# Performance work log

Hardware: AMD Instinct MI355X
Metric: run time of the kernel (lower is better)

Reference implementation:

```python
import jax, jax.numpy as jnp
import numpy as np

N = 50000      # nodes
F_IN = 128     # num_feat
HID = 128      # hidden size
OUT = 47       # num_out (classes)
E = 600000     # graph edges
EGO_E = 1200000  # concatenated egonet edges


def _linear_params(key, fan_in, fan_out):
    s = 1.0 / np.sqrt(fan_in)
    kw, kb = jax.random.split(key)
    W = jax.random.uniform(kw, (fan_in, fan_out), jnp.float32, -s, s)
    b = jax.random.uniform(kb, (fan_out,), jnp.float32, -s, s)
    return W, b


def setup_inputs() -> dict:
    key = jax.random.key(0)
    ks = jax.random.split(key, 8)
    x_in = jax.random.normal(ks[0], (N, F_IN), jnp.float32)
    edge_index_in = jax.random.randint(ks[1], (2, E), 0, N)
    ego_edge_index = jax.random.randint(ks[2], (2, EGO_E), 0, N)
    W_ego0, b_ego0 = _linear_params(ks[3], F_IN, F_IN)
    W_gin0, b_gin0 = _linear_params(ks[4], F_IN, HID)
    W_ego1, b_ego1 = _linear_params(ks[5], HID, HID)
    W_gin1, b_gin1 = _linear_params(ks[6], HID, OUT)
    return {
        "x_in": x_in, "edge_index_in": edge_index_in, "ego_edge_index": ego_edge_index,
        "W_ego0": W_ego0, "b_ego0": b_ego0, "W_gin0": W_gin0, "b_gin0": b_gin0,
        "W_ego1": W_ego1, "b_ego1": b_ego1, "W_gin1": W_gin1, "b_gin1": b_gin1,
    }


def reference(x_in, edge_index_in, ego_edge_index,
              W_ego0, b_ego0, W_gin0, b_gin0,
              W_ego1, b_ego1, W_gin1, b_gin1):
    n = x_in.shape[0]
    ego_row, ego_col = ego_edge_index[0], ego_edge_index[1]
    src, tgt = edge_index_in[0], edge_index_in[1]

    def do_conv(x):
        # sum_i spmm(A_i, x) == scatter-add over concatenated egonet edges, then / N
        return jax.ops.segment_sum(x[ego_col], ego_row, num_segments=n) * (1.0 / n)

    def gin(x, W, b):
        # GINConv(nn=Linear), eps=0: Linear(x + sum_{j->i} x_j)
        aggr = jax.ops.segment_sum(x[src], tgt, num_segments=n)
        return (x + aggr) @ W + b

    # layer 0: ['Ego','GIN', relu_mid=True, relu_end=True]
    x = do_conv(x_in) @ W_ego0 + b_ego0
    x = jax.nn.relu(x)
    x = gin(x, W_gin0, b_gin0)
    x = jax.nn.relu(x)
    # layer 1: ['Ego','GIN', relu_mid=True, relu_end=False]
    x = do_conv(x) @ W_ego1 + b_ego1
    x = jax.nn.relu(x)
    x = gin(x, W_gin1, b_gin1)
    return jax.nn.log_softmax(x, axis=1)
```

## Files before the change

kernel.cpp:

```cpp
#include <hip/hip_runtime.h>

#define SCAP_EGO 8192
#define SCAP_E   4096

typedef unsigned short ushort_t;
typedef unsigned int uint_t;
typedef __attribute__((ext_vector_type(8))) short bf16x8;
typedef __attribute__((ext_vector_type(4))) float f32x4;

__device__ inline float lo16(uint_t u) { return __uint_as_float(u << 16); }
__device__ inline float hi16(uint_t u) { return __uint_as_float(u & 0xFFFF0000u); }
__device__ inline ushort_t f2bf(float f) {
    uint_t i = __float_as_uint(f);
    return (ushort_t)((i + 0x7FFFu + ((i >> 16) & 1u)) >> 16);
}
__device__ inline uint_t pack2(float a, float b) {
    return (uint_t)f2bf(a) | ((uint_t)f2bf(b) << 16);
}

__global__ __launch_bounds__(256) void prep(
    const float* __restrict__ x, ushort_t* __restrict__ xb, int n8,
    const float* __restrict__ W0, const float* __restrict__ W1,
    const float* __restrict__ W2, const float* __restrict__ W3,
    ushort_t* __restrict__ T0, ushort_t* __restrict__ T1,
    ushort_t* __restrict__ T2, ushort_t* __restrict__ T3,
    int* __restrict__ z)
{
    int i = blockIdx.x * 256 + threadIdx.x;
    if (i < 128) ((int4*)z)[i] = make_int4(0, 0, 0, 0);
    if (i < n8) {
        const float4* p = (const float4*)(x + (size_t)i * 8);
        float4 a = p[0], b = p[1];
        uint4 o;
        o.x = pack2(a.x, a.y); o.y = pack2(a.z, a.w);
        o.z = pack2(b.x, b.y); o.w = pack2(b.z, b.w);
        *(uint4*)(xb + (size_t)i * 8) = o;
    }
    if (i < 49152) {
        int mi = i >> 14;
        int r = i & 16383;
        int n = r >> 7, k = r & 127;
        const float* W = mi == 0 ? W0 : (mi == 1 ? W1 : W2);
        ushort_t* T = mi == 0 ? T0 : (mi == 1 ? T1 : T2);
        T[n * 128 + k] = f2bf(W[k * 128 + n]);
    } else if (i < 49152 + 6144) {
        int r = i - 49152;
        int n = r >> 7, k = r & 127;
        T3[n * 128 + k] = (n < 47) ? f2bf(W3[k * 47 + n]) : (ushort_t)0;
    }
}

__global__ __launch_bounds__(256) void bin_edges2(
    const int* __restrict__ d1, const int* __restrict__ s1, int n1, int nb1,
    int* __restrict__ cur1, int2* __restrict__ st1, int scap1,
    const int* __restrict__ d2, const int* __restrict__ s2, int n2,
    int* __restrict__ cur2, int2* __restrict__ st2, int scap2)
{
    const int* dst; const int* src; int nE, scap; int* bincur; int2* stage; int bid;
    if (blockIdx.x < (uint_t)nb1) {
        dst = d1; src = s1; nE = n1; scap = scap1; bincur = cur1; stage = st1;
        bid = blockIdx.x;
    } else {
        dst = d2; src = s2; nE = n2; scap = scap2; bincur = cur2; stage = st2;
        bid = blockIdx.x - nb1;
    }
    __shared__ int bcnt[256];
    __shared__ int gbase[256];
    int t = threadIdx.x;
    bcnt[t] = 0;
    __syncthreads();
    int base = bid * 4096;
    int d[16], s[16], l[16];
#pragma unroll
    for (int i = 0; i < 16; i++) {
        int e = base + t + i * 256;
        if (e < nE) {
            d[i] = dst[e]; s[i] = src[e];
            l[i] = atomicAdd(&bcnt[d[i] >> 8], 1);
        } else d[i] = -1;
    }
    __syncthreads();
    if (bcnt[t]) gbase[t] = atomicAdd(&bincur[t], bcnt[t]);
    __syncthreads();
#pragma unroll
    for (int i = 0; i < 16; i++) {
        if (d[i] >= 0) {
            int b = d[i] >> 8;
            int slot = gbase[b] + l[i];
            if (slot < scap) stage[(size_t)b * scap + slot] = make_int2(d[i], s[i]);
        }
    }
}

__global__ __launch_bounds__(256) void build_csr2(
    const int* __restrict__ cur1, const int2* __restrict__ st1, int scap1,
    int* __restrict__ cnt1, int* __restrict__ rp1, int* __restrict__ pk1,
    const int* __restrict__ cur2, const int2* __restrict__ st2, int scap2,
    int* __restrict__ cnt2, int* __restrict__ rp2, int* __restrict__ pk2,
    int NB)
{
    const int* bincur; const int2* stage; int scap;
    int* cnt; int* rowptr; int* packed; int b;
    if (blockIdx.x < (uint_t)NB) {
        bincur = cur1; stage = st1; scap = scap1;
        cnt = cnt1; rowptr = rp1; packed = pk1; b = blockIdx.x;
    } else {
        bincur = cur2; stage = st2; scap = scap2;
        cnt = cnt2; rowptr = rp2; packed = pk2; b = blockIdx.x - NB;
    }
    __shared__ int sc[256];
    __shared__ int wcur[256];
    int t = threadIdx.x;
    int m = bincur[b]; if (m > scap) m = scap;
    const int2* st = stage + (size_t)b * scap;
    sc[t] = 0;
    __syncthreads();
    for (int e = t; e < m; e += 256) atomicAdd(&sc[st[e].x & 255], 1);
    __syncthreads();
    int v = sc[t];
    __syncthreads();
    sc[t] = v;
    __syncthreads();
    for (int off = 1; off < 256; off <<= 1) {
        int y = (t >= off) ? sc[t - off] : 0;
        __syncthreads();
        sc[t] += y;
        __syncthreads();
    }
    int excl = sc[t] - v;
    cnt[b * 256 + t] = v;
    rowptr[b * 256 + t] = b * scap + excl;
    wcur[t] = excl;
    __syncthreads();
    int* pk = packed + (size_t)b * scap;
    for (int e = t; e < m; e += 256) {
        int2 p = st[e];
        int slot = atomicAdd(&wcur[p.x & 255], 1);
        pk[slot] = p.y;
    }
}

template<int SELF>
__global__ __launch_bounds__(256, 8) void fused16(
    const ushort_t* __restrict__ X,
    const int* __restrict__ cnt, const int* __restrict__ rowptr,
    const int* __restrict__ packed,
    const ushort_t* __restrict__ WT, const float* __restrict__ bias,
    ushort_t* __restrict__ outb, int nrows, float scale)
{
    __shared__ ushort_t As[16][136];
    int t = threadIdx.x;
    int g = t >> 4, lane = t & 15;
    int blockBase = blockIdx.x * 16;
    int n = blockBase + g;
    const ushort_t* base = X + lane * 8;
    float a[8];
#pragma unroll
    for (int i = 0; i < 8; i++) a[i] = 0.f;
    if (n < nrows) {
        int len = cnt[n];
        const int* row = packed + rowptr[n];
        int e = 0;
        for (; e + 3 < len; e += 4) {
            uint4 w0 = *(const uint4*)(base + (size_t)row[e] * 128);
            uint4 w1 = *(const uint4*)(base + (size_t)row[e + 1] * 128);
            uint4 w2 = *(const uint4*)(base + (size_t)row[e + 2] * 128);
            uint4 w3 = *(const uint4*)(base + (size_t)row[e + 3] * 128);
            a[0] += lo16(w0.x) + lo16(w1.x) + lo16(w2.x) + lo16(w3.x);
            a[1] += hi16(w0.x) + hi16(w1.x) + hi16(w2.x) + hi16(w3.x);
            a[2] += lo16(w0.y) + lo16(w1.y) + lo16(w2.y) + lo16(w3.y);
            a[3] += hi16(w0.y) + hi16(w1.y) + hi16(w2.y) + hi16(w3.y);
            a[4] += lo16(w0.z) + lo16(w1.z) + lo16(w2.z) + lo16(w3.z);
            a[5] += hi16(w0.z) + hi16(w1.z) + hi16(w2.z) + hi16(w3.z);
            a[6] += lo16(w0.w) + lo16(w1.w) + lo16(w2.w) + lo16(w3.w);
            a[7] += hi16(w0.w) + hi16(w1.w) + hi16(w2.w) + hi16(w3.w);
        }
        for (; e < len; e++) {
            uint4 w = *(const uint4*)(base + (size_t)row[e] * 128);
            a[0] += lo16(w.x); a[1] += hi16(w.x);
            a[2] += lo16(w.y); a[3] += hi16(w.y);
            a[4] += lo16(w.z); a[5] += hi16(w.z);
            a[6] += lo16(w.w); a[7] += hi16(w.w);
        }
        if (SELF) {
            uint4 w = *(const uint4*)(base + (size_t)n * 128);
            a[0] += lo16(w.x); a[1] += hi16(w.x);
            a[2] += lo16(w.y); a[3] += hi16(w.y);
            a[4] += lo16(w.z); a[5] += hi16(w.z);
            a[6] += lo16(w.w); a[7] += hi16(w.w);
        }
    }
    uint4 o;
    o.x = pack2(a[0] * scale, a[1] * scale);
    o.y = pack2(a[2] * scale, a[3] * scale);
    o.z = pack2(a[4] * scale, a[5] * scale);
    o.w = pack2(a[6] * scale, a[7] * scale);
    *(uint4*)&As[g][lane * 8] = o;
    __syncthreads();
    int wave = t >> 6, l64 = t & 63;
    int m = l64 & 15, quad = l64 >> 4;
    bf16x8 afr[4];
#pragma unroll
    for (int kt = 0; kt < 4; kt++)
        afr[kt] = *(const bf16x8*)&As[m][kt * 32 + quad * 8];
    f32x4 acc[2];
#pragma unroll
    for (int j = 0; j < 2; j++) acc[j] = (f32x4){0.f, 0.f, 0.f, 0.f};
#pragma unroll
    for (int j = 0; j < 2; j++) {
        int ct = wave * 2 + j;
#pragma unroll
        for (int kt = 0; kt < 4; kt++) {
            bf16x8 b = *(const bf16x8*)(WT + (size_t)(ct * 16 + m) * 128
                                           + kt * 32 + quad * 8);
            acc[j] = __builtin_amdgcn_mfma_f32_16x16x32_bf16(afr[kt], b, acc[j], 0, 0, 0);
        }
    }
#pragma unroll
    for (int j = 0; j < 2; j++) {
        int col = (wave * 2 + j) * 16 + m;
        float bb = bias[col];
#pragma unroll
        for (int r = 0; r < 4; r++) {
            int row = blockBase + quad * 4 + r;
            if (row < nrows) {
                float v = acc[j][r] + bb;
                v = fmaxf(v, 0.f);
                outb[(size_t)row * 128 + col] = f2bf(v);
            }
        }
    }
}

__global__ __launch_bounds__(256, 8) void fused47(
    const ushort_t* __restrict__ X,
    const int* __restrict__ cnt, const int* __restrict__ rowptr,
    const int* __restrict__ packed,
    const ushort_t* __restrict__ WT, const float* __restrict__ bias,
    float* __restrict__ out, int nrows)
{
    __shared__ ushort_t As[16][136];
    int t = threadIdx.x;
    int g = t >> 4, lane = t & 15;
    int blockBase = blockIdx.x * 16;
    int n = blockBase + g;
    const ushort_t* base = X + lane * 8;
    float a[8];
#pragma unroll
    for (int i = 0; i < 8; i++) a[i] = 0.f;
    if (n < nrows) {
        int len = cnt[n];
        const int* row = packed + rowptr[n];
        int e = 0;
        for (; e + 3 < len; e += 4) {
            uint4 w0 = *(const uint4*)(base + (size_t)row[e] * 128);
            uint4 w1 = *(const uint4*)(base + (size_t)row[e + 1] * 128);
            uint4 w2 = *(const uint4*)(base + (size_t)row[e + 2] * 128);
            uint4 w3 = *(const uint4*)(base + (size_t)row[e + 3] * 128);
            a[0] += lo16(w0.x) + lo16(w1.x) + lo16(w2.x) + lo16(w3.x);
            a[1] += hi16(w0.x) + hi16(w1.x) + hi16(w2.x) + hi16(w3.x);
            a[2] += lo16(w0.y) + lo16(w1.y) + lo16(w2.y) + lo16(w3.y);
            a[3] += hi16(w0.y) + hi16(w1.y) + hi16(w2.y) + hi16(w3.y);
            a[4] += lo16(w0.z) + lo16(w1.z) + lo16(w2.z) + lo16(w3.z);
            a[5] += hi16(w0.z) + hi16(w1.z) + hi16(w2.z) + hi16(w3.z);
            a[6] += lo16(w0.w) + lo16(w1.w) + lo16(w2.w) + lo16(w3.w);
            a[7] += hi16(w0.w) + hi16(w1.w) + hi16(w2.w) + hi16(w3.w);
        }
        for (; e < len; e++) {
            uint4 w = *(const uint4*)(base + (size_t)row[e] * 128);
            a[0] += lo16(w.x); a[1] += hi16(w.x);
            a[2] += lo16(w.y); a[3] += hi16(w.y);
            a[4] += lo16(w.z); a[5] += hi16(w.z);
            a[6] += lo16(w.w); a[7] += hi16(w.w);
        }
        uint4 w = *(const uint4*)(base + (size_t)n * 128);
        a[0] += lo16(w.x); a[1] += hi16(w.x);
        a[2] += lo16(w.y); a[3] += hi16(w.y);
        a[4] += lo16(w.z); a[5] += hi16(w.z);
        a[6] += lo16(w.w); a[7] += hi16(w.w);
    }
    uint4 o;
    o.x = pack2(a[0], a[1]);
    o.y = pack2(a[2], a[3]);
    o.z = pack2(a[4], a[5]);
    o.w = pack2(a[6], a[7]);
    *(uint4*)&As[g][lane * 8] = o;
    __syncthreads();
    int wave = t >> 6;
    if (wave != 0) return;
    int l64 = t & 63;
    int m = l64 & 15, quad = l64 >> 4;
    bf16x8 afr[4];
#pragma unroll
    for (int kt = 0; kt < 4; kt++)
        afr[kt] = *(const bf16x8*)&As[m][kt * 32 + quad * 8];
    f32x4 acc[3];
#pragma unroll
    for (int ct = 0; ct < 3; ct++) acc[ct] = (f32x4){0.f, 0.f, 0.f, 0.f};
#pragma unroll
    for (int ct = 0; ct < 3; ct++) {
#pragma unroll
        for (int kt = 0; kt < 4; kt++) {
            bf16x8 b = *(const bf16x8*)(WT + (size_t)(ct * 16 + m) * 128
                                           + kt * 32 + quad * 8);
            acc[ct] = __builtin_amdgcn_mfma_f32_16x16x32_bf16(afr[kt], b, acc[ct], 0, 0, 0);
        }
    }
    int c0 = m, c1 = 16 + m, c2 = 32 + m;
    bool has2 = (c2 < 47);
    float b0 = bias[c0], b1 = bias[c1], b2 = has2 ? bias[c2] : 0.f;
#pragma unroll
    for (int r = 0; r < 4; r++) {
        int row = blockBase + quad * 4 + r;
        float v0 = acc[0][r] + b0;
        float v1 = acc[1][r] + b1;
        float v2 = has2 ? (acc[2][r] + b2) : -INFINITY;
        float mx = fmaxf(fmaxf(v0, v1), v2);
#pragma unroll
        for (int off = 8; off; off >>= 1) mx = fmaxf(mx, __shfl_xor(mx, off, 64));
        float s = __expf(v0 - mx) + __expf(v1 - mx) + (has2 ? __expf(v2 - mx) : 0.f);
#pragma unroll
        for (int off = 8; off; off >>= 1) s += __shfl_xor(s, off, 64);
        float lse = mx + __logf(s);
        if (row < nrows) {
            float* o2 = out + (size_t)row * 47;
            o2[c0] = v0 - lse;
            o2[c1] = v1 - lse;
            if (has2) o2[c2] = v2 - lse;
        }
    }
}

extern "C" void kernel_launch(void* const* d_in, const int* in_sizes, int n_in,
                              void* d_out, int out_size, void* d_ws, size_t ws_size,
                              hipStream_t stream) {
    const float* x_in   = (const float*)d_in[0];
    const int*   edge   = (const int*)d_in[1];
    const int*   ego    = (const int*)d_in[2];
    const float* W_ego0 = (const float*)d_in[3];
    const float* b_ego0 = (const float*)d_in[4];
    const float* W_gin0 = (const float*)d_in[5];
    const float* b_gin0 = (const float*)d_in[6];
    const float* W_ego1 = (const float*)d_in[7];
    const float* b_ego1 = (const float*)d_in[8];
    const float* W_gin1 = (const float*)d_in[9];
    const float* b_gin1 = (const float*)d_in[10];
    float* out = (float*)d_out;

    const int N     = in_sizes[0] / 128;
    const int E     = in_sizes[1] / 2;
    const int EGO_E = in_sizes[2] / 2;
    const float invN = 1.0f / (float)N;
    const int NB    = (N + 255) >> 8;

    const size_t NBELEM = (size_t)N * 128;
    ushort_t* Xb = (ushort_t*)d_ws;
    ushort_t* G  = Xb + NBELEM;
    ushort_t* H  = G + NBELEM;
    ushort_t* T0 = H + NBELEM;
    ushort_t* T1 = T0 + 16384;
    ushort_t* T2 = T1 + 16384;
    ushort_t* T3 = T2 + 16384;
    int* ip = (int*)(T3 + 6144);
    int* cnt_ego   = ip;             ip += NB * 256;
    int* rp_ego    = ip;             ip += NB * 256;
    int* cnt_edge  = ip;             ip += NB * 256;
    int* rp_edge   = ip;             ip += NB * 256;
    int* bincur    = ip;             ip += 512;
    int2* stage_ego  = (int2*)ip;    ip += (size_t)NB * SCAP_EGO * 2;
    int*  pk_ego     = ip;           ip += (size_t)NB * SCAP_EGO;
    int2* stage_edge = (int2*)ip;    ip += (size_t)NB * SCAP_E * 2;
    int*  pk_edge    = ip;           ip += (size_t)NB * SCAP_E;

    const int gFused  = (N + 15) / 16;
    const int gBinE   = (EGO_E + 4095) / 4096;
    const int gBinF   = (E + 4095) / 4096;
    const int gCvt    = ((N * 128 / 8) + 255) / 256;

    prep<<<gCvt, 256, 0, stream>>>(x_in, Xb, N * 128 / 8,
                                   W_ego0, W_gin0, W_ego1, W_gin1,
                                   T0, T1, T2, T3, bincur);
    bin_edges2<<<gBinE + gBinF, 256, 0, stream>>>(
        ego, ego + EGO_E, EGO_E, gBinE, bincur, stage_ego, SCAP_EGO,
        edge + E, edge, E, bincur + 256, stage_edge, SCAP_E);
    build_csr2<<<2 * NB, 256, 0, stream>>>(
        bincur, stage_ego, SCAP_EGO, cnt_ego, rp_ego, pk_ego,
        bincur + 256, stage_edge, SCAP_E, cnt_edge, rp_edge, pk_edge, NB);

    fused16<0><<<gFused, 256, 0, stream>>>(Xb, cnt_ego, rp_ego, pk_ego,
                                           T0, b_ego0, H, N, invN);
    fused16<1><<<gFused, 256, 0, stream>>>(H, cnt_edge, rp_edge, pk_edge,
                                           T1, b_gin0, G, N, 1.f);
    fused16<0><<<gFused, 256, 0, stream>>>(G, cnt_ego, rp_ego, pk_ego,
                                           T2, b_ego1, H, N, invN);
    fused47<<<gFused, 256, 0, stream>>>(H, cnt_edge, rp_edge, pk_edge,
                                        T3, b_gin1, out, N);
}
```

Baseline: 300.7 us.

## Fuse all pipeline stages into one persistent cooperative kernel with grid syncs

Replaces the seven separate launches (prep, edge binning, CSR build, and the four aggregate-plus-matmul stages) with a single cooperative kernel. Blocks loop over work items and separate stages with grid.sync. The grid size comes from the occupancy query, capped at 2048 blocks. This is meant to remove per-launch overhead and the tail idle time at kernel boundaries, at the cost of grid-wide barriers, one register budget shared by every stage (possible spills in the binning code under the 8-blocks-per-CU bound), and a fallback multi-kernel path if the cooperative launch fails.

```diff
diff --git a/kernel.cpp b/kernel.cpp
--- a/kernel.cpp
+++ b/kernel.cpp
@@ -1,4 +1,7 @@
 #include <hip/hip_runtime.h>
+#include <hip/hip_cooperative_groups.h>
+
+namespace cg = cooperative_groups;
 
 #define SCAP_EGO 8192
 #define SCAP_E   4096
@@ -18,7 +21,8 @@
     return (uint_t)f2bf(a) | ((uint_t)f2bf(b) << 16);
 }
 
-__global__ __launch_bounds__(256) void prep(
+
+__device__ __forceinline__ void dev_prep_item(int i,
     const float* __restrict__ x, ushort_t* __restrict__ xb, int n8,
     const float* __restrict__ W0, const float* __restrict__ W1,
     const float* __restrict__ W2, const float* __restrict__ W3,
@@ -26,7 +30,6 @@
     ushort_t* __restrict__ T2, ushort_t* __restrict__ T3,
     int* __restrict__ z)
 {
-    int i = blockIdx.x * 256 + threadIdx.x;
     if (i < 128) ((int4*)z)[i] = make_int4(0, 0, 0, 0);
     if (i < n8) {
         const float4* p = (const float4*)(x + (size_t)i * 8);
@@ -50,23 +53,21 @@
     }
 }
 
-__global__ __launch_bounds__(256) void bin_edges2(
-    const int* __restrict__ d1, const int* __restrict__ s1, int n1, int nb1,
-    int* __restrict__ cur1, int2* __restrict__ st1, int scap1,
+__device__ __forceinline__ void dev_bin_chunk(int c, int nc1,
+    const int* __restrict__ d1, const int* __restrict__ s1, int n1,
+    int2* __restrict__ st1, int* __restrict__ cur1, int scap1,
     const int* __restrict__ d2, const int* __restrict__ s2, int n2,
-    int* __restrict__ cur2, int2* __restrict__ st2, int scap2)
+    int2* __restrict__ st2, int* __restrict__ cur2, int scap2,
+    int* bcnt, int* gbase, int t)
 {
     const int* dst; const int* src; int nE, scap; int* bincur; int2* stage; int bid;
-    if (blockIdx.x < (uint_t)nb1) {
+    if (c < nc1) {
         dst = d1; src = s1; nE = n1; scap = scap1; bincur = cur1; stage = st1;
-        bid = blockIdx.x;
+        bid = c;
     } else {
         dst = d2; src = s2; nE = n2; scap = scap2; bincur = cur2; stage = st2;
-        bid = blockIdx.x - nb1;
-    }
-    __shared__ int bcnt[256];
-    __shared__ int gbase[256];
-    int t = threadIdx.x;
+        bid = c - nc1;
+    }
     bcnt[t] = 0;
     __syncthreads();
     int base = bid * 4096;
@@ -90,27 +91,25 @@
             if (slot < scap) stage[(size_t)b * scap + slot] = make_int2(d[i], s[i]);
         }
     }
-}
-
-__global__ __launch_bounds__(256) void build_csr2(
+    __syncthreads();
+}
+
+__device__ __forceinline__ void dev_csr_bin(int c, int NB,
     const int* __restrict__ cur1, const int2* __restrict__ st1, int scap1,
     int* __restrict__ cnt1, int* __restrict__ rp1, int* __restrict__ pk1,
     const int* __restrict__ cur2, const int2* __restrict__ st2, int scap2,
     int* __restrict__ cnt2, int* __restrict__ rp2, int* __restrict__ pk2,
-    int NB)
+    int* sc, int* wcur, int t)
 {
     const int* bincur; const int2* stage; int scap;
     int* cnt; int* rowptr; int* packed; int b;
-    if (blockIdx.x < (uint_t)NB) {
+    if (c < NB) {
         bincur = cur1; stage = st1; scap = scap1;
-        cnt = cnt1; rowptr = rp1; packed = pk1; b = blockIdx.x;
+        cnt = cnt1; rowptr = rp1; packed = pk1; b = c;
     } else {
         bincur = cur2; stage = st2; scap = scap2;
-        cnt = cnt2; rowptr = rp2; packed = pk2; b = blockIdx.x - NB;
-    }
-    __shared__ int sc[256];
-    __shared__ int wcur[256];
-    int t = threadIdx.x;
+        cnt = cnt2; rowptr = rp2; packed = pk2; b = c - NB;
+    }
     int m = bincur[b]; if (m > scap) m = scap;
     const int2* st = stage + (size_t)b * scap;
     sc[t] = 0;
@@ -134,24 +133,23 @@
     __syncthreads();
     int* pk = packed + (size_t)b * scap;
     for (int e = t; e < m; e += 256) {
-        int2 p = st[e];
-        int slot = atomicAdd(&wcur[p.x & 255], 1);
-        pk[slot] = p.y;
-    }
-}
-
-template<int SELF>
-__global__ __launch_bounds__(256, 8) void fused16(
+        int2 p2 = st[e];
+        int slot = atomicAdd(&wcur[p2.x & 255], 1);
+        pk[slot] = p2.y;
+    }
+    __syncthreads();
+}
+
+__device__ __forceinline__ void dev_f16(int tile, int SELF,
     const ushort_t* __restrict__ X,
     const int* __restrict__ cnt, const int* __restrict__ rowptr,
     const int* __restrict__ packed,
     const ushort_t* __restrict__ WT, const float* __restrict__ bias,
-    ushort_t* __restrict__ outb, int nrows, float scale)
-{
-    __shared__ ushort_t As[16][136];
-    int t = threadIdx.x;
+    ushort_t* __restrict__ outb, int nrows, float scale,
+    ushort_t As[16][136], int t)
+{
     int g = t >> 4, lane = t & 15;
-    int blockBase = blockIdx.x * 16;
+    int blockBase = tile * 16;
     int n = blockBase + g;
     const ushort_t* base = X + lane * 8;
     float a[8];
@@ -230,19 +228,19 @@
             }
         }
     }
-}
-
-__global__ __launch_bounds__(256, 8) void fused47(
+    __syncthreads();
+}
+
+__device__ __forceinline__ void dev_f47(int tile,
     const ushort_t* __restrict__ X,
     const int* __restrict__ cnt, const int* __restrict__ rowptr,
     const int* __restrict__ packed,
     const ushort_t* __restrict__ WT, const float* __restrict__ bias,
-    float* __restrict__ out, int nrows)
-{
-    __shared__ ushort_t As[16][136];
-    int t = threadIdx.x;
+    float* __restrict__ out, int nrows,
+    ushort_t As[16][136], int t)
+{
     int g = t >> 4, lane = t & 15;
-    int blockBase = blockIdx.x * 16;
+    int blockBase = tile * 16;
     int n = blockBase + g;
     const ushort_t* base = X + lane * 8;
     float a[8];
@@ -287,48 +285,153 @@
     *(uint4*)&As[g][lane * 8] = o;
     __syncthreads();
     int wave = t >> 6;
-    if (wave != 0) return;
-    int l64 = t & 63;
-    int m = l64 & 15, quad = l64 >> 4;
-    bf16x8 afr[4];
-#pragma unroll
-    for (int kt = 0; kt < 4; kt++)
-        afr[kt] = *(const bf16x8*)&As[m][kt * 32 + quad * 8];
-    f32x4 acc[3];
-#pragma unroll
-    for (int ct = 0; ct < 3; ct++) acc[ct] = (f32x4){0.f, 0.f, 0.f, 0.f};
-#pragma unroll
-    for (int ct = 0; ct < 3; ct++) {
-#pragma unroll
-        for (int kt = 0; kt < 4; kt++) {
-            bf16x8 b = *(const bf16x8*)(WT + (size_t)(ct * 16 + m) * 128
-                                           + kt * 32 + quad * 8);
-            acc[ct] = __builtin_amdgcn_mfma_f32_16x16x32_bf16(afr[kt], b, acc[ct], 0, 0, 0);
-        }
-    }
-    int c0 = m, c1 = 16 + m, c2 = 32 + m;
-    bool has2 = (c2 < 47);
-    float b0 = bias[c0], b1 = bias[c1], b2 = has2 ? bias[c2] : 0.f;
-#pragma unroll
-    for (int r = 0; r < 4; r++) {
-        int row = blockBase + quad * 4 + r;
-        float v0 = acc[0][r] + b0;
-        float v1 = acc[1][r] + b1;
-        float v2 = has2 ? (acc[2][r] + b2) : -INFINITY;
-        float mx = fmaxf(fmaxf(v0, v1), v2);
-#pragma unroll
-        for (int off = 8; off; off >>= 1) mx = fmaxf(mx, __shfl_xor(mx, off, 64));
-        float s = __expf(v0 - mx) + __expf(v1 - mx) + (has2 ? __expf(v2 - mx) : 0.f);
-#pragma unroll
-        for (int off = 8; off; off >>= 1) s += __shfl_xor(s, off, 64);
-        float lse = mx + __logf(s);
-        if (row < nrows) {
-            float* o2 = out + (size_t)row * 47;
-            o2[c0] = v0 - lse;
-            o2[c1] = v1 - lse;
-            if (has2) o2[c2] = v2 - lse;
-        }
-    }
+    if (wave == 0) {
+        int l64 = t & 63;
+        int m = l64 & 15, quad = l64 >> 4;
+        bf16x8 afr[4];
+#pragma unroll
+        for (int kt = 0; kt < 4; kt++)
+            afr[kt] = *(const bf16x8*)&As[m][kt * 32 + quad * 8];
+        f32x4 acc[3];
+#pragma unroll
+        for (int ct = 0; ct < 3; ct++) acc[ct] = (f32x4){0.f, 0.f, 0.f, 0.f};
+#pragma unroll
+        for (int ct = 0; ct < 3; ct++) {
+#pragma unroll
+            for (int kt = 0; kt < 4; kt++) {
+                bf16x8 b = *(const bf16x8*)(WT + (size_t)(ct * 16 + m) * 128
+                                               + kt * 32 + quad * 8);
+                acc[ct] = __builtin_amdgcn_mfma_f32_16x16x32_bf16(afr[kt], b, acc[ct], 0, 0, 0);
+            }
+        }
+        int c0 = m, c1 = 16 + m, c2 = 32 + m;
+        bool has2 = (c2 < 47);
+        float b0 = bias[c0], b1 = bias[c1], b2 = has2 ? bias[c2] : 0.f;
+#pragma unroll
+        for (int r = 0; r < 4; r++) {
+            int row = blockBase + quad * 4 + r;
+            float v0 = acc[0][r] + b0;
+            float v1 = acc[1][r] + b1;
+            float v2 = has2 ? (acc[2][r] + b2) : -INFINITY;
+            float mx = fmaxf(fmaxf(v0, v1), v2);
+#pragma unroll
+            for (int off = 8; off; off >>= 1) mx = fmaxf(mx, __shfl_xor(mx, off, 64));
+            float s = __expf(v0 - mx) + __expf(v1 - mx) + (has2 ? __expf(v2 - mx) : 0.f);
+#pragma unroll
+            for (int off = 8; off; off >>= 1) s += __shfl_xor(s, off, 64);
+            float lse = mx + __logf(s);
+            if (row < nrows) {
+                float* o2 = out + (size_t)row * 47;
+                o2[c0] = v0 - lse;
+                o2[c1] = v1 - lse;
+                if (has2) o2[c2] = v2 - lse;
+            }
+        }
+    }
+    __syncthreads();
+}
+
+struct MegaP {
+    const float* x_in; const int* edge; const int* ego;
+    const float *W0, *W1, *W2, *W3;
+    const float *bE0, *bG0, *bE1, *bG1;
+    float* out;
+    ushort_t *Xb, *G, *H, *T0, *T1, *T2, *T3;
+    int *cnt_ego, *rp_ego, *pk_ego, *cnt_edge, *rp_edge, *pk_edge, *bincur;
+    int2 *st_ego, *st_edge;
+    int N, E, EGO_E, NB, n8; float invN;
+};
+
+__global__ __launch_bounds__(256, 8) void mega(MegaP p)
+{
+    cg::grid_group grid = cg::this_grid();
+    __shared__ int sA[256], sB[256];
+    __shared__ ushort_t As[16][136];
+    int t = threadIdx.x, bid = blockIdx.x, nb = gridDim.x;
+    int gsz = nb * 256, tix = bid * 256 + t;
+
+    for (int i = tix; i < p.n8; i += gsz)
+        dev_prep_item(i, p.x_in, p.Xb, p.n8, p.W0, p.W1, p.W2, p.W3,
+                      p.T0, p.T1, p.T2, p.T3, p.bincur);
+    grid.sync();
+
+    int nc1 = (p.EGO_E + 4095) >> 12, nc2 = (p.E + 4095) >> 12;
+    for (int c = bid; c < nc1 + nc2; c += nb)
+        dev_bin_chunk(c, nc1,
+                      p.ego, p.ego + p.EGO_E, p.EGO_E, p.st_ego, p.bincur, SCAP_EGO,
+                      p.edge + p.E, p.edge, p.E, p.st_edge, p.bincur + 256, SCAP_E,
+                      sA, sB, t);
+    grid.sync();
+
+    for (int c = bid; c < 2 * p.NB; c += nb)
+        dev_csr_bin(c, p.NB,
+                    p.bincur, p.st_ego, SCAP_EGO, p.cnt_ego, p.rp_ego, p.pk_ego,
+                    p.bincur + 256, p.st_edge, SCAP_E, p.cnt_edge, p.rp_edge, p.pk_edge,
+                    sA, sB, t);
+    grid.sync();
+
+    int nt = (p.N + 15) >> 4;
+    for (int tile = bid; tile < nt; tile += nb)
+        dev_f16(tile, 0, p.Xb, p.cnt_ego, p.rp_ego, p.pk_ego,
+                p.T0, p.bE0, p.H, p.N, p.invN, As, t);
+    grid.sync();
+    for (int tile = bid; tile < nt; tile += nb)
+        dev_f16(tile, 1, p.H, p.cnt_edge, p.rp_edge, p.pk_edge,
+                p.T1, p.bG0, p.G, p.N, 1.f, As, t);
+    grid.sync();
+    for (int tile = bid; tile < nt; tile += nb)
+        dev_f16(tile, 0, p.G, p.cnt_ego, p.rp_ego, p.pk_ego,
+                p.T2, p.bE1, p.H, p.N, p.invN, As, t);
+    grid.sync();
+    for (int tile = bid; tile < nt; tile += nb)
+        dev_f47(tile, p.H, p.cnt_edge, p.rp_edge, p.pk_edge,
+                p.T3, p.bG1, p.out, p.N, As, t);
+}
+
+__global__ __launch_bounds__(256) void k_prep(
+    const float* x, ushort_t* xb, int n8,
+    const float* W0, const float* W1, const float* W2, const float* W3,
+    ushort_t* T0, ushort_t* T1, ushort_t* T2, ushort_t* T3, int* z)
+{
+    int i = blockIdx.x * 256 + threadIdx.x;
+    dev_prep_item(i, x, xb, n8, W0, W1, W2, W3, T0, T1, T2, T3, z);
+}
+
+__global__ __launch_bounds__(256) void k_bin(
+    const int* d1, const int* s1, int n1, int nb1, int* cur1, int2* st1, int scap1,
+    const int* d2, const int* s2, int n2, int* cur2, int2* st2, int scap2)
+{
+    __shared__ int bcnt[256], gbase[256];
+    dev_bin_chunk(blockIdx.x, nb1, d1, s1, n1, st1, cur1, scap1,
+                  d2, s2, n2, st2, cur2, scap2, bcnt, gbase, threadIdx.x);
+}
+
+__global__ __launch_bounds__(256) void k_csr(
+    const int* cur1, const int2* st1, int scap1, int* cnt1, int* rp1, int* pk1,
+    const int* cur2, const int2* st2, int scap2, int* cnt2, int* rp2, int* pk2,
+    int NB)
+{
+    __shared__ int sc[256], wcur[256];
+    dev_csr_bin(blockIdx.x, NB, cur1, st1, scap1, cnt1, rp1, pk1,
+                cur2, st2, scap2, cnt2, rp2, pk2, sc, wcur, threadIdx.x);
+}
+
+__global__ __launch_bounds__(256, 8) void k_f16(
+    const ushort_t* X, const int* cnt, const int* rp, const int* pk,
+    const ushort_t* WT, const float* bias, ushort_t* outb, int nrows,
+    float scale, int SELF)
+{
+    __shared__ ushort_t As[16][136];
+    dev_f16(blockIdx.x, SELF, X, cnt, rp, pk, WT, bias, outb, nrows, scale,
+            As, threadIdx.x);
+}
+
+__global__ __launch_bounds__(256, 8) void k_f47(
+    const ushort_t* X, const int* cnt, const int* rp, const int* pk,
+    const ushort_t* WT, const float* bias, float* out, int nrows)
+{
+    __shared__ ushort_t As[16][136];
+    dev_f47(blockIdx.x, X, cnt, rp, pk, WT, bias, out, nrows, As, threadIdx.x);
 }
 
 extern "C" void kernel_launch(void* const* d_in, const int* in_sizes, int n_in,
@@ -352,6 +455,7 @@
     const int EGO_E = in_sizes[2] / 2;
     const float invN = 1.0f / (float)N;
     const int NB    = (N + 255) >> 8;
+    const int n8    = N * 128 / 8;
 
     const size_t NBELEM = (size_t)N * 128;
     ushort_t* Xb = (ushort_t*)d_ws;
@@ -372,27 +476,61 @@
     int2* stage_edge = (int2*)ip;    ip += (size_t)NB * SCAP_E * 2;
     int*  pk_edge    = ip;           ip += (size_t)NB * SCAP_E;
 
-    const int gFused  = (N + 15) / 16;
-    const int gBinE   = (EGO_E + 4095) / 4096;
-    const int gBinF   = (E + 4095) / 4096;
-    const int gCvt    = ((N * 128 / 8) + 255) / 256;
-
-    prep<<<gCvt, 256, 0, stream>>>(x_in, Xb, N * 128 / 8,
-                                   W_ego0, W_gin0, W_ego1, W_gin1,
-                                   T0, T1, T2, T3, bincur);
-    bin_edges2<<<gBinE + gBinF, 256, 0, stream>>>(
-        ego, ego + EGO_E, EGO_E, gBinE, bincur, stage_ego, SCAP_EGO,
-        edge + E, edge, E, bincur + 256, stage_edge, SCAP_E);
-    build_csr2<<<2 * NB, 256, 0, stream>>>(
-        bincur, stage_ego, SCAP_EGO, cnt_ego, rp_ego, pk_ego,
-        bincur + 256, stage_edge, SCAP_E, cnt_edge, rp_edge, pk_edge, NB);
-
-    fused16<0><<<gFused, 256, 0, stream>>>(Xb, cnt_ego, rp_ego, pk_ego,
-                                           T0, b_ego0, H, N, invN);
-    fused16<1><<<gFused, 256, 0, stream>>>(H, cnt_edge, rp_edge, pk_edge,
-                                           T1, b_gin0, G, N, 1.f);
-    fused16<0><<<gFused, 256, 0, stream>>>(G, cnt_ego, rp_ego, pk_ego,
-                                           T2, b_ego1, H, N, invN);
-    fused47<<<gFused, 256, 0, stream>>>(H, cnt_edge, rp_edge, pk_edge,
-                                        T3, b_gin1, out, N);
-}
+    MegaP P;
+    P.x_in = x_in; P.edge = edge; P.ego = ego;
+    P.W0 = W_ego0; P.W1 = W_gin0; P.W2 = W_ego1; P.W3 = W_gin1;
+    P.bE0 = b_ego0; P.bG0 = b_gin0; P.bE1 = b_ego1; P.bG1 = b_gin1;
+    P.out = out;
+    P.Xb = Xb; P.G = G; P.H = H;
+    P.T0 = T0; P.T1 = T1; P.T2 = T2; P.T3 = T3;
+    P.cnt_ego = cnt_ego; P.rp_ego = rp_ego; P.pk_ego = pk_ego;
+    P.cnt_edge = cnt_edge; P.rp_edge = rp_edge; P.pk_edge = pk_edge;
+    P.bincur = bincur; P.st_ego = stage_ego; P.st_edge = stage_edge;
+    P.N = N; P.E = E; P.EGO_E = EGO_E; P.NB = NB; P.n8 = n8; P.invN = invN;
+
+    static int coopGrid = 0;
+    if (coopGrid == 0) {
+        int dev = 0; (void)hipGetDevice(&dev);
+        hipDeviceProp_t prop;
+        int nCU = 256;
+        if (hipGetDeviceProperties(&prop, dev) == hipSuccess &&
+            prop.multiProcessorCount > 0)
+            nCU = prop.multiProcessorCount;
+        int mab = 0;
+        if (hipOccupancyMaxActiveBlocksPerMultiprocessor(&mab, mega, 256, 0)
+                != hipSuccess || mab < 1)
+            mab = 1;
+        long g = (long)mab * nCU;
+        if (g > 2048) g = 2048;
+        coopGrid = (int)g;
+    }
+
+    void* kargs[] = { (void*)&P };
+    hipError_t err = hipLaunchCooperativeKernel((const void*)mega,
+                                                dim3(coopGrid), dim3(256),
+                                                kargs, 0, stream);
+    if (err != hipSuccess) {
+        (void)hipGetLastError();
+        const int gFused = (N + 15) / 16;
+        const int gBinE  = (EGO_E + 4095) / 4096;
+        const int gBinF  = (E + 4095) / 4096;
+        const int gCvt   = (n8 + 255) / 256;
+        k_prep<<<gCvt, 256, 0, stream>>>(x_in, Xb, n8,
+                                         W_ego0, W_gin0, W_ego1, W_gin1,
+                                         T0, T1, T2, T3, bincur);
+        k_bin<<<gBinE + gBinF, 256, 0, stream>>>(
+            ego, ego + EGO_E, EGO_E, gBinE, bincur, stage_ego, SCAP_EGO,
+            edge + E, edge, E, bincur + 256, stage_edge, SCAP_E);
+        k_csr<<<2 * NB, 256, 0, stream>>>(
+            bincur, stage_ego, SCAP_EGO, cnt_ego, rp_ego, pk_ego,
+            bincur + 256, stage_edge, SCAP_E, cnt_edge, rp_edge, pk_edge, NB);
+        k_f16<<<gFused, 256, 0, stream>>>(Xb, cnt_ego, rp_ego, pk_ego,
+                                          T0, b_ego0, H, N, invN, 0);
+        k_f16<<<gFused, 256, 0, stream>>>(H, cnt_edge, rp_edge, pk_edge,
+                                          T1, b_gin0, G, N, 1.f, 1);
+        k_f16<<<gFused, 256, 0, stream>>>(G, cnt_ego, rp_ego, pk_ego,
+                                          T2, b_ego1, H, N, invN, 0);
+        k_f47<<<gFused, 256, 0, stream>>>(H, cnt_edge, rp_edge, pk_edge,
+                                          T3, b_gin1, out, N);
+    }
+}
```

New measurement: 1.125 ms. 3.74x slower.

## Merge prep, edge binning and CSR build into one persistent kernel with grid barrier

Applied to the files above, without the earlier changes.

Replaces the three separate preprocessing launches (bf16 conversion, edge binning, CSR build) with one persistent kernel of 896 blocks. It uses a software grid barrier between the binning and CSR phases, plus a tiny zeroing kernel for the counters. It also hoists the weight-fragment loads in fused16 ahead of the shared-memory barrier so they overlap with the aggregation store. The aim is to cut kernel launch gaps and tail effects. The grid barrier relies on all 896 blocks being co-resident, which risks deadlock if occupancy is lower.

```diff
diff --git a/kernel.cpp b/kernel.cpp
--- a/kernel.cpp
+++ b/kernel.cpp
@@ -18,16 +18,38 @@
     return (uint_t)f2bf(a) | ((uint_t)f2bf(b) << 16);
 }
 
-__global__ __launch_bounds__(256) void prep(
+__global__ __launch_bounds__(256) void zeroK(int* __restrict__ z)
+{
+    for (int i = threadIdx.x; i < 516; i += 256) z[i] = 0;
+}
+
+__device__ __forceinline__ void grid_barrier(int* bar, int* gen, int t)
+{
+    __threadfence();
+    __syncthreads();
+    if (t == 0) {
+        int g = __hip_atomic_load(gen, __ATOMIC_RELAXED, __HIP_MEMORY_SCOPE_AGENT);
+        int a = __hip_atomic_fetch_add(bar, 1, __ATOMIC_ACQ_REL, __HIP_MEMORY_SCOPE_AGENT);
+        if (a == (int)gridDim.x - 1) {
+            __hip_atomic_store(bar, 0, __ATOMIC_RELAXED, __HIP_MEMORY_SCOPE_AGENT);
+            __hip_atomic_store(gen, g + 1, __ATOMIC_RELEASE, __HIP_MEMORY_SCOPE_AGENT);
+        } else {
+            while (__hip_atomic_load(gen, __ATOMIC_ACQUIRE, __HIP_MEMORY_SCOPE_AGENT) == g)
+                __builtin_amdgcn_s_sleep(2);
+        }
+    }
+    __syncthreads();
+    __threadfence();
+}
+
+
+__device__ __forceinline__ void dev_prep_item(int i,
     const float* __restrict__ x, ushort_t* __restrict__ xb, int n8,
     const float* __restrict__ W0, const float* __restrict__ W1,
     const float* __restrict__ W2, const float* __restrict__ W3,
     ushort_t* __restrict__ T0, ushort_t* __restrict__ T1,
-    ushort_t* __restrict__ T2, ushort_t* __restrict__ T3,
-    int* __restrict__ z)
-{
-    int i = blockIdx.x * 256 + threadIdx.x;
-    if (i < 128) ((int4*)z)[i] = make_int4(0, 0, 0, 0);
+    ushort_t* __restrict__ T2, ushort_t* __restrict__ T3)
+{
     if (i < n8) {
         const float4* p = (const float4*)(x + (size_t)i * 8);
         float4 a = p[0], b = p[1];
@@ -50,23 +72,21 @@
     }
 }
 
-__global__ __launch_bounds__(256) void bin_edges2(
-    const int* __restrict__ d1, const int* __restrict__ s1, int n1, int nb1,
-    int* __restrict__ cur1, int2* __restrict__ st1, int scap1,
+__device__ __forceinline__ void dev_bin_chunk(int c, int nc1,
+    const int* __restrict__ d1, const int* __restrict__ s1, int n1,
+    int2* __restrict__ st1, int* __restrict__ cur1, int scap1,
     const int* __restrict__ d2, const int* __restrict__ s2, int n2,
-    int* __restrict__ cur2, int2* __restrict__ st2, int scap2)
+    int2* __restrict__ st2, int* __restrict__ cur2, int scap2,
+    int* bcnt, int* gbase, int t)
 {
     const int* dst; const int* src; int nE, scap; int* bincur; int2* stage; int bid;
-    if (blockIdx.x < (uint_t)nb1) {
+    if (c < nc1) {
         dst = d1; src = s1; nE = n1; scap = scap1; bincur = cur1; stage = st1;
-        bid = blockIdx.x;
+        bid = c;
     } else {
         dst = d2; src = s2; nE = n2; scap = scap2; bincur = cur2; stage = st2;
-        bid = blockIdx.x - nb1;
-    }
-    __shared__ int bcnt[256];
-    __shared__ int gbase[256];
-    int t = threadIdx.x;
+        bid = c - nc1;
+    }
     bcnt[t] = 0;
     __syncthreads();
     int base = bid * 4096;
@@ -90,27 +110,25 @@
             if (slot < scap) stage[(size_t)b * scap + slot] = make_int2(d[i], s[i]);
         }
     }
-}
-
-__global__ __launch_bounds__(256) void build_csr2(
+    __syncthreads();
+}
+
+__device__ __forceinline__ void dev_csr_bin(int c, int NB,
     const int* __restrict__ cur1, const int2* __restrict__ st1, int scap1,
     int* __restrict__ cnt1, int* __restrict__ rp1, int* __restrict__ pk1,
     const int* __restrict__ cur2, const int2* __restrict__ st2, int scap2,
     int* __restrict__ cnt2, int* __restrict__ rp2, int* __restrict__ pk2,
-    int NB)
+    int* sc, int* wcur, int t)
 {
     const int* bincur; const int2* stage; int scap;
     int* cnt; int* rowptr; int* packed; int b;
-    if (blockIdx.x < (uint_t)NB) {
+    if (c < NB) {
         bincur = cur1; stage = st1; scap = scap1;
-        cnt = cnt1; rowptr = rp1; packed = pk1; b = blockIdx.x;
+        cnt = cnt1; rowptr = rp1; packed = pk1; b = c;
     } else {
         bincur = cur2; stage = st2; scap = scap2;
-        cnt = cnt2; rowptr = rp2; packed = pk2; b = blockIdx.x - NB;
-    }
-    __shared__ int sc[256];
-    __shared__ int wcur[256];
-    int t = threadIdx.x;
+        cnt = cnt2; rowptr = rp2; packed = pk2; b = c - NB;
+    }
     int m = bincur[b]; if (m > scap) m = scap;
     const int2* st = stage + (size_t)b * scap;
     sc[t] = 0;
@@ -134,10 +152,48 @@
     __syncthreads();
     int* pk = packed + (size_t)b * scap;
     for (int e = t; e < m; e += 256) {
-        int2 p = st[e];
-        int slot = atomicAdd(&wcur[p.x & 255], 1);
-        pk[slot] = p.y;
-    }
+        int2 p2 = st[e];
+        int slot = atomicAdd(&wcur[p2.x & 255], 1);
+        pk[slot] = p2.y;
+    }
+    __syncthreads();
+}
+
+__global__ __launch_bounds__(256) void graphbuild(
+    const float* __restrict__ x, ushort_t* __restrict__ xb, int n8,
+    const float* __restrict__ W0, const float* __restrict__ W1,
+    const float* __restrict__ W2, const float* __restrict__ W3,
+    ushort_t* __restrict__ T0, ushort_t* __restrict__ T1,
+    ushort_t* __restrict__ T2, ushort_t* __restrict__ T3,
+    const int* __restrict__ ego, int nEgo,
+    const int* __restrict__ edge, int nEdge,
+    int* __restrict__ bincur,
+    int2* __restrict__ st_ego, int2* __restrict__ st_edge,
+    int* __restrict__ cnt_ego, int* __restrict__ rp_ego, int* __restrict__ pk_ego,
+    int* __restrict__ cnt_edge, int* __restrict__ rp_edge, int* __restrict__ pk_edge,
+    int NB, int* __restrict__ bar, int* __restrict__ gen)
+{
+    __shared__ int sA[256], sB[256];
+    int t = threadIdx.x, bid = blockIdx.x;
+    int gsz = gridDim.x * 256;
+
+    for (int i = bid * 256 + t; i < n8; i += gsz)
+        dev_prep_item(i, x, xb, n8, W0, W1, W2, W3, T0, T1, T2, T3);
+
+    int nc1 = (nEgo + 4095) >> 12, nc2 = (nEdge + 4095) >> 12;
+    for (int c = bid; c < nc1 + nc2; c += gridDim.x)
+        dev_bin_chunk(c, nc1,
+                      ego, ego + nEgo, nEgo, st_ego, bincur, SCAP_EGO,
+                      edge + nEdge, edge, nEdge, st_edge, bincur + 256, SCAP_E,
+                      sA, sB, t);
+
+    grid_barrier(bar, gen, t);
+
+    for (int c = bid; c < 2 * NB; c += gridDim.x)
+        dev_csr_bin(c, NB,
+                    bincur, st_ego, SCAP_EGO, cnt_ego, rp_ego, pk_ego,
+                    bincur + 256, st_edge, SCAP_E, cnt_edge, rp_edge, pk_edge,
+                    sA, sB, t);
 }
 
 template<int SELF>
@@ -196,9 +252,18 @@
     o.z = pack2(a[4] * scale, a[5] * scale);
     o.w = pack2(a[6] * scale, a[7] * scale);
     *(uint4*)&As[g][lane * 8] = o;
-    __syncthreads();
     int wave = t >> 6, l64 = t & 63;
     int m = l64 & 15, quad = l64 >> 4;
+    bf16x8 bfr[2][4];
+#pragma unroll
+    for (int j = 0; j < 2; j++) {
+        int ct = wave * 2 + j;
+#pragma unroll
+        for (int kt = 0; kt < 4; kt++)
+            bfr[j][kt] = *(const bf16x8*)(WT + (size_t)(ct * 16 + m) * 128
+                                             + kt * 32 + quad * 8);
+    }
+    __syncthreads();
     bf16x8 afr[4];
 #pragma unroll
     for (int kt = 0; kt < 4; kt++)
@@ -208,13 +273,9 @@
     for (int j = 0; j < 2; j++) acc[j] = (f32x4){0.f, 0.f, 0.f, 0.f};
 #pragma unroll
     for (int j = 0; j < 2; j++) {
-        int ct = wave * 2 + j;
-#pragma unroll
-        for (int kt = 0; kt < 4; kt++) {
-            bf16x8 b = *(const bf16x8*)(WT + (size_t)(ct * 16 + m) * 128
-                                           + kt * 32 + quad * 8);
-            acc[j] = __builtin_amdgcn_mfma_f32_16x16x32_bf16(afr[kt], b, acc[j], 0, 0, 0);
-        }
+#pragma unroll
+        for (int kt = 0; kt < 4; kt++)
+            acc[j] = __builtin_amdgcn_mfma_f32_16x16x32_bf16(afr[kt], bfr[j][kt], acc[j], 0, 0, 0);
     }
 #pragma unroll
     for (int j = 0; j < 2; j++) {
@@ -352,6 +413,7 @@
     const int EGO_E = in_sizes[2] / 2;
     const float invN = 1.0f / (float)N;
     const int NB    = (N + 255) >> 8;
+    const int n8    = N * 128 / 8;
 
     const size_t NBELEM = (size_t)N * 128;
     ushort_t* Xb = (ushort_t*)d_ws;
@@ -367,26 +429,23 @@
     int* cnt_edge  = ip;             ip += NB * 256;
     int* rp_edge   = ip;             ip += NB * 256;
     int* bincur    = ip;             ip += 512;
+    int* bar       = ip;             ip += 2;
+    ip += 2;
     int2* stage_ego  = (int2*)ip;    ip += (size_t)NB * SCAP_EGO * 2;
     int*  pk_ego     = ip;           ip += (size_t)NB * SCAP_EGO;
     int2* stage_edge = (int2*)ip;    ip += (size_t)NB * SCAP_E * 2;
     int*  pk_edge    = ip;           ip += (size_t)NB * SCAP_E;
 
-    const int gFused  = (N + 15) / 16;
-    const int gBinE   = (EGO_E + 4095) / 4096;
-    const int gBinF   = (E + 4095) / 4096;
-    const int gCvt    = ((N * 128 / 8) + 255) / 256;
-
-    prep<<<gCvt, 256, 0, stream>>>(x_in, Xb, N * 128 / 8,
-                                   W_ego0, W_gin0, W_ego1, W_gin1,
-                                   T0, T1, T2, T3, bincur);
-    bin_edges2<<<gBinE + gBinF, 256, 0, stream>>>(
-        ego, ego + EGO_E, EGO_E, gBinE, bincur, stage_ego, SCAP_EGO,
-        edge + E, edge, E, bincur + 256, stage_edge, SCAP_E);
-    build_csr2<<<2 * NB, 256, 0, stream>>>(
-        bincur, stage_ego, SCAP_EGO, cnt_ego, rp_ego, pk_ego,
-        bincur + 256, stage_edge, SCAP_E, cnt_edge, rp_edge, pk_edge, NB);
-
+    const int gFused = (N + 15) / 16;
+    const int gBuild = 896;
+
+    zeroK<<<1, 256, 0, stream>>>(bincur);
+    graphbuild<<<gBuild, 256, 0, stream>>>(
+        x_in, Xb, n8, W_ego0, W_gin0, W_ego1, W_gin1, T0, T1, T2, T3,
+        ego, EGO_E, edge, E, bincur,
+        stage_ego, stage_edge,
+        cnt_ego, rp_ego, pk_ego, cnt_edge, rp_edge, pk_edge,
+        NB, bar, bar + 1);
     fused16<0><<<gFused, 256, 0, stream>>>(Xb, cnt_ego, rp_ego, pk_ego,
                                            T0, b_ego0, H, N, invN);
     fused16<1><<<gFused, 256, 0, stream>>>(H, cnt_edge, rp_edge, pk_edge,
```

Result: slower. 714.1 us (+137.5%).

## Sort rows by degree within bins to balance gather work across blocks

Applied to the files above, without the earlier changes.

build_csr2 now does a counting sort of the 256 rows in each bin by in-degree (capped at 255) and writes a permutation. The fused kernels process rows in that order, so the 16 rows in a block have similar degrees, which cuts intra-block divergence and imbalance during the neighbour gather. Output rows are scattered through a shared-memory copy of the permutation, and the grid grows to cover the padded NB*256 rows. The first weight fragment is also loaded before the barrier to overlap with the gather. Costs are an extra scan in CSR build, an indirection per row, and loss of spatial locality in writes and self-loads.

```diff
diff --git a/kernel.cpp b/kernel.cpp
--- a/kernel.cpp
+++ b/kernel.cpp
@@ -95,18 +95,20 @@
 __global__ __launch_bounds__(256) void build_csr2(
     const int* __restrict__ cur1, const int2* __restrict__ st1, int scap1,
     int* __restrict__ cnt1, int* __restrict__ rp1, int* __restrict__ pk1,
+    int* __restrict__ perm1,
     const int* __restrict__ cur2, const int2* __restrict__ st2, int scap2,
     int* __restrict__ cnt2, int* __restrict__ rp2, int* __restrict__ pk2,
+    int* __restrict__ perm2,
     int NB)
 {
     const int* bincur; const int2* stage; int scap;
-    int* cnt; int* rowptr; int* packed; int b;
+    int* cnt; int* rowptr; int* packed; int* perm; int b;
     if (blockIdx.x < (uint_t)NB) {
         bincur = cur1; stage = st1; scap = scap1;
-        cnt = cnt1; rowptr = rp1; packed = pk1; b = blockIdx.x;
+        cnt = cnt1; rowptr = rp1; packed = pk1; perm = perm1; b = blockIdx.x;
     } else {
         bincur = cur2; stage = st2; scap = scap2;
-        cnt = cnt2; rowptr = rp2; packed = pk2; b = blockIdx.x - NB;
+        cnt = cnt2; rowptr = rp2; packed = pk2; perm = perm2; b = blockIdx.x - NB;
     }
     __shared__ int sc[256];
     __shared__ int wcur[256];
@@ -138,21 +140,43 @@
         int slot = atomicAdd(&wcur[p.x & 255], 1);
         pk[slot] = p.y;
     }
+    __syncthreads();
+    sc[t] = 0;
+    __syncthreads();
+    int dcap = v > 255 ? 255 : v;
+    atomicAdd(&sc[dcap], 1);
+    __syncthreads();
+    int h = sc[t];
+    __syncthreads();
+    sc[t] = h;
+    __syncthreads();
+    for (int off = 1; off < 256; off <<= 1) {
+        int y = (t >= off) ? sc[t - off] : 0;
+        __syncthreads();
+        sc[t] += y;
+        __syncthreads();
+    }
+    wcur[t] = sc[t] - h;
+    __syncthreads();
+    int rank = atomicAdd(&wcur[dcap], 1);
+    perm[b * 256 + rank] = b * 256 + t;
 }
 
 template<int SELF>
 __global__ __launch_bounds__(256, 8) void fused16(
     const ushort_t* __restrict__ X,
     const int* __restrict__ cnt, const int* __restrict__ rowptr,
-    const int* __restrict__ packed,
+    const int* __restrict__ packed, const int* __restrict__ perm,
     const ushort_t* __restrict__ WT, const float* __restrict__ bias,
     ushort_t* __restrict__ outb, int nrows, float scale)
 {
     __shared__ ushort_t As[16][136];
+    __shared__ int sP[16];
     int t = threadIdx.x;
     int g = t >> 4, lane = t & 15;
     int blockBase = blockIdx.x * 16;
-    int n = blockBase + g;
+    int n = perm[blockBase + g];
+    if (lane == 0) sP[g] = n;
     const ushort_t* base = X + lane * 8;
     float a[8];
 #pragma unroll
@@ -196,9 +220,14 @@
     o.z = pack2(a[4] * scale, a[5] * scale);
     o.w = pack2(a[6] * scale, a[7] * scale);
     *(uint4*)&As[g][lane * 8] = o;
-    __syncthreads();
     int wave = t >> 6, l64 = t & 63;
     int m = l64 & 15, quad = l64 >> 4;
+    bf16x8 bfr0[4];
+#pragma unroll
+    for (int kt = 0; kt < 4; kt++)
+        bfr0[kt] = *(const bf16x8*)(WT + (size_t)((wave * 2) * 16 + m) * 128
+                                       + kt * 32 + quad * 8);
+    __syncthreads();
     bf16x8 afr[4];
 #pragma unroll
     for (int kt = 0; kt < 4; kt++)
@@ -207,14 +236,13 @@
 #pragma unroll
     for (int j = 0; j < 2; j++) acc[j] = (f32x4){0.f, 0.f, 0.f, 0.f};
 #pragma unroll
-    for (int j = 0; j < 2; j++) {
-        int ct = wave * 2 + j;
-#pragma unroll
-        for (int kt = 0; kt < 4; kt++) {
-            bf16x8 b = *(const bf16x8*)(WT + (size_t)(ct * 16 + m) * 128
-                                           + kt * 32 + quad * 8);
-            acc[j] = __builtin_amdgcn_mfma_f32_16x16x32_bf16(afr[kt], b, acc[j], 0, 0, 0);
-        }
+    for (int kt = 0; kt < 4; kt++)
+        acc[0] = __builtin_amdgcn_mfma_f32_16x16x32_bf16(afr[kt], bfr0[kt], acc[0], 0, 0, 0);
+#pragma unroll
+    for (int kt = 0; kt < 4; kt++) {
+        bf16x8 b = *(const bf16x8*)(WT + (size_t)((wave * 2 + 1) * 16 + m) * 128
+                                       + kt * 32 + quad * 8);
+        acc[1] = __builtin_amdgcn_mfma_f32_16x16x32_bf16(afr[kt], b, acc[1], 0, 0, 0);
     }
 #pragma unroll
     for (int j = 0; j < 2; j++) {
@@ -222,11 +250,11 @@
         float bb = bias[col];
 #pragma unroll
         for (int r = 0; r < 4; r++) {
-            int row = blockBase + quad * 4 + r;
-            if (row < nrows) {
+            int rr = sP[quad * 4 + r];
+            if (rr < nrows) {
                 float v = acc[j][r] + bb;
                 v = fmaxf(v, 0.f);
-                outb[(size_t)row * 128 + col] = f2bf(v);
+                outb[(size_t)rr * 128 + col] = f2bf(v);
             }
         }
     }
@@ -235,15 +263,17 @@
 __global__ __launch_bounds__(256, 8) void fused47(
     const ushort_t* __restrict__ X,
     const int* __restrict__ cnt, const int* __restrict__ rowptr,
-    const int* __restrict__ packed,
+    const int* __restrict__ packed, const int* __restrict__ perm,
     const ushort_t* __restrict__ WT, const float* __restrict__ bias,
     float* __restrict__ out, int nrows)
 {
     __shared__ ushort_t As[16][136];
+    __shared__ int sP[16];
     int t = threadIdx.x;
     int g = t >> 4, lane = t & 15;
     int blockBase = blockIdx.x * 16;
-    int n = blockBase + g;
+    int n = perm[blockBase + g];
+    if (lane == 0) sP[g] = n;
     const ushort_t* base = X + lane * 8;
     float a[8];
 #pragma unroll
@@ -311,7 +341,7 @@
     float b0 = bias[c0], b1 = bias[c1], b2 = has2 ? bias[c2] : 0.f;
 #pragma unroll
     for (int r = 0; r < 4; r++) {
-        int row = blockBase + quad * 4 + r;
+        int rr = sP[quad * 4 + r];
         float v0 = acc[0][r] + b0;
         float v1 = acc[1][r] + b1;
         float v2 = has2 ? (acc[2][r] + b2) : -INFINITY;
@@ -322,8 +352,8 @@
 #pragma unroll
         for (int off = 8; off; off >>= 1) s += __shfl_xor(s, off, 64);
         float lse = mx + __logf(s);
-        if (row < nrows) {
-            float* o2 = out + (size_t)row * 47;
+        if (rr < nrows) {
+            float* o2 = out + (size_t)rr * 47;
             o2[c0] = v0 - lse;
             o2[c1] = v1 - lse;
             if (has2) o2[c2] = v2 - lse;
@@ -366,13 +396,15 @@
     int* rp_ego    = ip;             ip += NB * 256;
     int* cnt_edge  = ip;             ip += NB * 256;
     int* rp_edge   = ip;             ip += NB * 256;
+    int* perm_ego  = ip;             ip += NB * 256;
+    int* perm_edge = ip;             ip += NB * 256;
     int* bincur    = ip;             ip += 512;
     int2* stage_ego  = (int2*)ip;    ip += (size_t)NB * SCAP_EGO * 2;
     int*  pk_ego     = ip;           ip += (size_t)NB * SCAP_EGO;
     int2* stage_edge = (int2*)ip;    ip += (size_t)NB * SCAP_E * 2;
     int*  pk_edge    = ip;           ip += (size_t)NB * SCAP_E;
 
-    const int gFused  = (N + 15) / 16;
+    const int gFused  = NB * 16;
     const int gBinE   = (EGO_E + 4095) / 4096;
     const int gBinF   = (E + 4095) / 4096;
     const int gCvt    = ((N * 128 / 8) + 255) / 256;
@@ -384,15 +416,16 @@
         ego, ego + EGO_E, EGO_E, gBinE, bincur, stage_ego, SCAP_EGO,
         edge + E, edge, E, bincur + 256, stage_edge, SCAP_E);
     build_csr2<<<2 * NB, 256, 0, stream>>>(
-        bincur, stage_ego, SCAP_EGO, cnt_ego, rp_ego, pk_ego,
-        bincur + 256, stage_edge, SCAP_E, cnt_edge, rp_edge, pk_edge, NB);
-
-    fused16<0><<<gFused, 256, 0, stream>>>(Xb, cnt_ego, rp_ego, pk_ego,
+        bincur, stage_ego, SCAP_EGO, cnt_ego, rp_ego, pk_ego, perm_ego,
+        bincur + 256, stage_edge, SCAP_E, cnt_edge, rp_edge, pk_edge, perm_edge,
+        NB);
+
+    fused16<0><<<gFused, 256, 0, stream>>>(Xb, cnt_ego, rp_ego, pk_ego, perm_ego,
                                            T0, b_ego0, H, N, invN);
-    fused16<1><<<gFused, 256, 0, stream>>>(H, cnt_edge, rp_edge, pk_edge,
+    fused16<1><<<gFused, 256, 0, stream>>>(H, cnt_edge, rp_edge, pk_edge, perm_edge,
                                            T1, b_gin0, G, N, 1.f);
-    fused16<0><<<gFused, 256, 0, stream>>>(G, cnt_ego, rp_ego, pk_ego,
+    fused16<0><<<gFused, 256, 0, stream>>>(G, cnt_ego, rp_ego, pk_ego, perm_ego,
                                            T2, b_ego1, H, N, invN);
-    fused47<<<gFused, 256, 0, stream>>>(H, cnt_edge, rp_edge, pk_edge,
+    fused47<<<gFused, 256, 0, stream>>>(H, cnt_edge, rp_edge, pk_edge, perm_edge,
                                         T3, b_gin1, out, N);
 }
```

Result: slower. 309.6 us (+3.0%).
